# Kernel tuning notes

Hardware: AMD Instinct MI355X
Metric: run time of the kernel (lower is better)

## Reference

```python
import jax, jax.numpy as jnp
import numpy as np

EPS = 1e-12  # torch F.normalize eps

def l2norm(x, axis):
    n = jnp.sqrt(jnp.sum(x * x, axis=axis, keepdims=True))
    return x / jnp.maximum(n, EPS)

def setup_inputs() -> dict:
    key = jax.random.key(0)
    k1, k2, k3, k4 = jax.random.split(key, 4)
    N, C, H, W, K = 128, 128, 64, 64, 64
    x = jax.random.normal(k1, (N, C, H, W), dtype=jnp.float32)
    conv_w = jax.random.normal(k2, (K, C), dtype=jnp.float32) * 0.1
    conv_b = jax.random.normal(k3, (K,), dtype=jnp.float32) * 0.1
    centroids = jax.random.uniform(k4, (K, C), dtype=jnp.float32)
    return {"x": x, "conv_w": conv_w, "conv_b": conv_b, "centroids": centroids}

def reference(x, conv_w, conv_b, centroids):
    N, C, H, W = x.shape
    K = centroids.shape[0]
    xf = x.reshape(N, C, H * W)               # [N, C, S]
    xf = l2norm(xf, axis=1)                   # normalize_input over channels
    # 1x1 conv -> logits [N, K, S], softmax over clusters
    logits = jnp.einsum('ncs,kc->nks', xf, conv_w) + conv_b[None, :, None]
    a = jax.nn.softmax(logits, axis=1)        # [N, K, S]
    # VLAD: sum_s a[n,k,s]*(x[n,:,s] - c[k]) = (a @ x^T) - (sum_s a) * c
    vlad = jnp.einsum('nks,ncs->nkc', a, xf) - a.sum(axis=-1)[:, :, None] * centroids[None]
    vlad = l2norm(vlad, axis=2)               # intra-normalization
    vlad = vlad.reshape(N, K * C)
    return l2norm(vlad, axis=1)
```

## Files before the change

### kernel.cpp

```cpp
#include <hip/hip_runtime.h>
#include <math.h>

#define N_IMG 128
#define C_DIM 128
#define K_CL  64
#define S_PIX 4096
#define PB    4
#define SPB   (S_PIX/PB)
#define CHK   32
#define NCHK  (SPB/CHK)
#define NBUF  4

typedef __attribute__((ext_vector_type(8))) short bf16x8;
typedef __attribute__((ext_vector_type(4))) float f32x4;

__device__ __forceinline__ unsigned short f2bf_rn(float v) {
    unsigned u = __float_as_uint(v);
    unsigned r = u + 0x7fffu + ((u >> 16) & 1u);
    return (unsigned short)(r >> 16);
}
__device__ __forceinline__ float bf2f(unsigned short h) {
    return __uint_as_float(((unsigned)h) << 16);
}

__device__ __forceinline__ int sx(int c) { return ((c & 3) | ((c & 1) << 2)) & 7; }
__device__ __forceinline__ int sa(int k) { return (k >> 2) & 3; }

__device__ __forceinline__ void cvt8(const float* v, bf16x8& h, bf16x8& l) {
    union { unsigned w[4]; bf16x8 v8; } H, L;
    #pragma unroll
    for (int p = 0; p < 4; ++p) {
        unsigned u0 = __float_as_uint(v[2*p]);
        unsigned u1 = __float_as_uint(v[2*p+1]);
        float r0 = v[2*p]   - __uint_as_float(u0 & 0xffff0000u);
        float r1 = v[2*p+1] - __uint_as_float(u1 & 0xffff0000u);
        H.w[p] = __builtin_amdgcn_perm(u1, u0, 0x07060302u);
        L.w[p] = __builtin_amdgcn_perm(__float_as_uint(r1), __float_as_uint(r0), 0x07060302u);
    }
    h = H.v8; l = L.v8;
}

__device__ __forceinline__ void gll16(const float* g, float* l) {
    __builtin_amdgcn_global_load_lds(
        (const __attribute__((address_space(1))) unsigned int*)(g),
        (__attribute__((address_space(3))) unsigned int*)(l),
        16, 0, 0);
}

__global__ void k_prep(const float* __restrict__ w, unsigned short* __restrict__ wf,
                       float4* __restrict__ out4, float4* __restrict__ asum4) {
    int i = blockIdx.x * 256 + threadIdx.x;
    f32x4 z = (f32x4)0.f;
    if (i < (N_IMG*K_CL*C_DIM)/4) out4[i] = *(float4*)&z;
    if (i < (N_IMG*K_CL)/4)       asum4[i] = *(float4*)&z;
    if (i < 8192) {
        int j = i & 7, l = (i >> 3) & 63, t = (i >> 9) & 3, m = (i >> 11) & 3;
        int k = 16*m + (l & 15);
        int c = 32*t + 4*j + (l >> 4);
        float v = w[k * C_DIM + c];
        unsigned short h = f2bf_rn(v);
        wf[i]        = h;
        wf[8192 + i] = f2bf_rn(v - bf2f(h));
    }
}

__global__ __launch_bounds__(256, 1)
void k_main(const float* __restrict__ x,
            const unsigned short* __restrict__ wf,
            const float* __restrict__ bias,
            float* __restrict__ vlad,
            float* __restrict__ asum)
{
    __shared__ float Xs[NBUF][C_DIM*CHK];
    __shared__ unsigned short aS[2*K_CL*CHK];
    __shared__ __align__(16) float redS[2][2][16];

    const int tid  = threadIdx.x;
    const int lane = tid & 63;
    const int wid  = tid >> 6;
    const int lc   = lane & 15;
    const int g    = lane >> 4;

    const int p  = wid & 1;
    const int mh = wid >> 1;
    const int px = p*16 + lc;
    const int cq = wid * 32;

    const int n  = blockIdx.x / PB;
    const int sp = blockIdx.x % PB;
    const float* xn = x + (size_t)n * (C_DIM * S_PIX) + sp * SPB;

    bf16x8 Wh[2][4], Wl[2][4];
    #pragma unroll
    for (int mm = 0; mm < 2; ++mm)
        #pragma unroll
        for (int t = 0; t < 4; ++t) {
            int m = 2*mh + mm;
            Wh[mm][t] = *(const bf16x8*)&wf[((m*4 + t)*64 + lane)*8];
            Wl[mm][t] = *(const bf16x8*)&wf[((16 + m*4 + t)*64 + lane)*8];
        }
    #pragma unroll
    for (int mm = 0; mm < 2; ++mm)
        #pragma unroll
        for (int t = 0; t < 4; ++t) {
            asm volatile("" : "+v"(Wh[mm][t]));
            asm volatile("" : "+v"(Wl[mm][t]));
        }
    f32x4 bias_r[2];
    #pragma unroll
    for (int mm = 0; mm < 2; ++mm)
        bias_r[mm] = *(const f32x4*)&bias[32*mh + 16*mm + 4*g];

    f32x4 accV[4][2];
    #pragma unroll
    for (int m = 0; m < 4; ++m) { accV[m][0] = (f32x4)0.f; accV[m][1] = (f32x4)0.f; }
    float asum_acc[8];
    #pragma unroll
    for (int i = 0; i < 8; ++i) asum_acc[i] = 0.f;

    const int eA  = g*32 + (((px >> 2) ^ sx(g)) << 2) + (px & 3);
    const int sxB = sx(lc);
    const int saB = sa(lc);
    const int ps  = g >> 1;
    const int sb  = (8*g) & 15;

    auto STAGE = [&](int t, float* Xbuf) {
        #pragma unroll
        for (int i2 = 0; i2 < 4; ++i2) {
            int rowblk = wid*32 + i2*8;
            int row = rowblk + (lane >> 3);
            const float* gp = xn + (size_t)row * S_PIX + t*CHK
                            + 4*((lane & 7) ^ sx(row));
            gll16(gp, &Xbuf[rowblk * 32]);
        }
    };

    STAGE(0, Xs[0]);
    STAGE(1, Xs[1]);
    STAGE(2, Xs[2]);
    asm volatile("s_waitcnt vmcnt(8)" ::: "memory");
    __builtin_amdgcn_s_barrier();
    __builtin_amdgcn_sched_barrier(0);

    for (int ch = 0; ch < NCHK; ++ch) {
        float* Xb = Xs[ch & (NBUF-1)];

        if (ch + 3 < NCHK) STAGE(ch + 3, Xs[(ch + 3) & (NBUF-1)]);

        float s0 = 0.f, s1 = 0.f, s2 = 0.f, s3 = 0.f;
        f32x4 accL[2];
        accL[0] = (f32x4)0.f; accL[1] = (f32x4)0.f;
        #pragma unroll
        for (int t = 0; t < 4; ++t) {
            float xv[8];
            #pragma unroll
            for (int j = 0; j < 8; ++j)
                xv[j] = Xb[eA + 1024*t + 128*j];
            s0 = fmaf(xv[0], xv[0], s0); s1 = fmaf(xv[1], xv[1], s1);
            s2 = fmaf(xv[2], xv[2], s2); s3 = fmaf(xv[3], xv[3], s3);
            s0 = fmaf(xv[4], xv[4], s0); s1 = fmaf(xv[5], xv[5], s1);
            s2 = fmaf(xv[6], xv[6], s2); s3 = fmaf(xv[7], xv[7], s3);
            bf16x8 xh, xl;
            cvt8(xv, xh, xl);
            #pragma unroll
            for (int mm = 0; mm < 2; ++mm) {
                accL[mm] = __builtin_amdgcn_mfma_f32_16x16x32_bf16(Wh[mm][t], xh, accL[mm], 0,0,0);
                accL[mm] = __builtin_amdgcn_mfma_f32_16x16x32_bf16(Wh[mm][t], xl, accL[mm], 0,0,0);
                accL[mm] = __builtin_amdgcn_mfma_f32_16x16x32_bf16(Wl[mm][t], xh, accL[mm], 0,0,0);
            }
        }
        float ss = (s0 + s1) + (s2 + s3);
        ss += __shfl_xor(ss, 16); ss += __shfl_xor(ss, 32);
        float rnorm = 1.0f / fmaxf(sqrtf(ss), 1e-12f);

        float e[8]; float sm = 0.f;
        #pragma unroll
        for (int mm = 0; mm < 2; ++mm)
            #pragma unroll
            for (int jj = 0; jj < 4; ++jj) {
                float t2 = __expf(fmaf(accL[mm][jj], rnorm, bias_r[mm][jj]));
                e[mm*4+jj] = t2;
                sm += t2;
            }
        sm += __shfl_xor(sm, 16); sm += __shfl_xor(sm, 32);
        if (g == 0) redS[p][mh][lc] = sm;

        #pragma unroll
        for (int mm = 0; mm < 2; ++mm)
            #pragma unroll
            for (int jj = 0; jj < 4; ++jj) {
                float ap = e[mm*4+jj] * rnorm;
                unsigned u = __float_as_uint(ap);
                float r = ap - __uint_as_float(u & 0xffff0000u);
                int k  = 32*mh + 16*mm + 4*g + jj;
                int ix = k*32 + (((px >> 3) ^ g) << 3) + (px & 7);
                aS[ix]        = (unsigned short)(u >> 16);
                aS[2048 + ix] = (unsigned short)(__float_as_uint(r) >> 16);
            }

        asm volatile("s_waitcnt lgkmcnt(0)" ::: "memory");
        __builtin_amdgcn_s_barrier();
        __builtin_amdgcn_sched_barrier(0);

        {
            float S = sm + redS[p][mh^1][lc];
            float coef = __builtin_amdgcn_rcpf(S);
            #pragma unroll
            for (int i = 0; i < 8; ++i) asum_acc[i] = fmaf(e[i], coef, asum_acc[i]);
        }

        {
            float4 u0 = *(const float4*)&redS[ps][0][sb];
            float4 u1 = *(const float4*)&redS[ps][0][sb+4];
            float4 v0 = *(const float4*)&redS[ps][1][sb];
            float4 v1 = *(const float4*)&redS[ps][1][sb+4];
            float cf[8] = {u0.x+v0.x, u0.y+v0.y, u0.z+v0.z, u0.w+v0.w,
                           u1.x+v1.x, u1.y+v1.y, u1.z+v1.z, u1.w+v1.w};
            #pragma unroll
            for (int j = 0; j < 8; ++j) cf[j] = __builtin_amdgcn_rcpf(cf[j]);

            bf16x8 Ah[4], Al[4];
            #pragma unroll
            for (int m = 0; m < 4; ++m) {
                int off = (16*m + lc)*32 + ((g ^ saB) << 3);
                Ah[m] = *(const bf16x8*)&aS[off];
                Al[m] = *(const bf16x8*)&aS[2048 + off];
            }
            #pragma unroll
            for (int nn = 0; nn < 2; ++nn) {
                int c  = cq + nn*16 + lc;
                int P0 = (2*g) ^ sxB;
                float4 f0 = *(const float4*)&Xb[c*32 + P0*4];
                float4 f1 = *(const float4*)&Xb[c*32 + (P0 ^ 1)*4];
                float xv[8] = {f0.x*cf[0], f0.y*cf[1], f0.z*cf[2], f0.w*cf[3],
                               f1.x*cf[4], f1.y*cf[5], f1.z*cf[6], f1.w*cf[7]};
                bf16x8 xh, xl;
                cvt8(xv, xh, xl);
                #pragma unroll
                for (int m = 0; m < 4; ++m) {
                    accV[m][nn] = __builtin_amdgcn_mfma_f32_16x16x32_bf16(Ah[m], xh, accV[m][nn], 0,0,0);
                    accV[m][nn] = __builtin_amdgcn_mfma_f32_16x16x32_bf16(Ah[m], xl, accV[m][nn], 0,0,0);
                    accV[m][nn] = __builtin_amdgcn_mfma_f32_16x16x32_bf16(Al[m], xh, accV[m][nn], 0,0,0);
                }
            }
        }

        if (ch + 1 < NCHK) {
            if (ch + 3 < NCHK)
                asm volatile("s_waitcnt vmcnt(8) lgkmcnt(0)" ::: "memory");
            else if (ch + 2 < NCHK)
                asm volatile("s_waitcnt vmcnt(4) lgkmcnt(0)" ::: "memory");
            else
                asm volatile("s_waitcnt vmcnt(0) lgkmcnt(0)" ::: "memory");
            __builtin_amdgcn_s_barrier();
            __builtin_amdgcn_sched_barrier(0);
        }
    }

    float* vb = vlad + (size_t)n * (K_CL * C_DIM);
    #pragma unroll
    for (int m = 0; m < 4; ++m)
        #pragma unroll
        for (int nn = 0; nn < 2; ++nn)
            #pragma unroll
            for (int jj = 0; jj < 4; ++jj)
                atomicAdd(&vb[(16*m + 4*g + jj)*C_DIM + cq + nn*16 + lc],
                          accV[m][nn][jj]);

    #pragma unroll
    for (int i = 0; i < 8; ++i) {
        float v = asum_acc[i];
        v += __shfl_xor(v, 1); v += __shfl_xor(v, 2);
        v += __shfl_xor(v, 4); v += __shfl_xor(v, 8);
        asum_acc[i] = v;
    }
    if (lc == 0) {
        #pragma unroll
        for (int mm = 0; mm < 2; ++mm)
            #pragma unroll
            for (int jj = 0; jj < 4; ++jj)
                atomicAdd(&asum[n*K_CL + 32*mh + 16*mm + 4*g + jj], asum_acc[mm*4+jj]);
    }
}

__global__ __launch_bounds__(256)
void k_final(float* __restrict__ vlad,
             const float* __restrict__ asum,
             const float* __restrict__ cent)
{
    __shared__ float v[K_CL * 132];
    __shared__ float red[K_CL][4];
    __shared__ float rin[K_CL];
    __shared__ float rtot_s;
    const int tid = threadIdx.x;
    const int n   = blockIdx.x;
    float* vb = vlad + (size_t)n * (K_CL * C_DIM);
    const float* as = asum + n * K_CL;

    for (int i4 = tid; i4 < (K_CL*C_DIM)/4; i4 += 256) {
        int k = i4 >> 5, c4 = i4 & 31;
        float4 a = *(const float4*)&vb[i4*4];
        float4 b = *(const float4*)&cent[i4*4];
        float ak = as[k];
        float4 r; r.x = a.x - ak*b.x; r.y = a.y - ak*b.y;
                  r.z = a.z - ak*b.z; r.w = a.w - ak*b.w;
        *(float4*)&v[k*132 + c4*4] = r;
    }
    __syncthreads();
    {
        int k = tid >> 2, p = tid & 3;
        float s2 = 0.f;
        #pragma unroll
        for (int u = 0; u < 32; ++u) { float t = v[k*132 + (u<<2) + p]; s2 = fmaf(t, t, s2); }
        red[k][p] = s2;
    }
    __syncthreads();
    if (tid < K_CL) {
        float s2 = red[tid][0] + red[tid][1] + red[tid][2] + red[tid][3];
        float r  = 1.0f / fmaxf(sqrtf(s2), 1e-12f);
        rin[tid] = r;
        red[tid][0] = s2 * r * r;
    }
    __syncthreads();
    if (tid < 64) {
        float t = red[tid][0];
        t += __shfl_xor(t, 32); t += __shfl_xor(t, 16); t += __shfl_xor(t, 8);
        t += __shfl_xor(t, 4);  t += __shfl_xor(t, 2);  t += __shfl_xor(t, 1);
        if (tid == 0) rtot_s = 1.0f / fmaxf(sqrtf(t), 1e-12f);
    }
    __syncthreads();
    float rt = rtot_s;
    for (int i4 = tid; i4 < (K_CL*C_DIM)/4; i4 += 256) {
        int k = i4 >> 5, c4 = i4 & 31;
        float4 a = *(const float4*)&v[k*132 + c4*4];
        float s = rin[k] * rt;
        float4 r; r.x = a.x*s; r.y = a.y*s; r.z = a.z*s; r.w = a.w*s;
        *(float4*)&vb[i4*4] = r;
    }
}

extern "C" void kernel_launch(void* const* d_in, const int* in_sizes, int n_in,
                              void* d_out, int out_size, void* d_ws, size_t ws_size,
                              hipStream_t stream) {
    const float* x    = (const float*)d_in[0];
    const float* w    = (const float*)d_in[1];
    const float* b    = (const float*)d_in[2];
    const float* cent = (const float*)d_in[3];
    float* out = (float*)d_out;
    unsigned short* wf = (unsigned short*)d_ws;
    float* asum = (float*)((char*)d_ws + 32768);

    k_prep<<<(N_IMG*K_CL*C_DIM/4 + 255)/256, 256, 0, stream>>>(
        w, wf, (float4*)out, (float4*)asum);
    k_main<<<N_IMG * PB, 256, 0, stream>>>(x, wf, b, out, asum);
    k_final<<<N_IMG, 256, 0, stream>>>(out, asum, cent);
}
```

Before: 105.2 us.

## Replace atomic VLAD accumulation with per-block partial buffers reduced in final kernel

Each main-kernel block now writes its partial VLAD and assignment-sum accumulators to its own workspace slice with plain vector stores, instead of issuing scalar atomicAdds into the output. The final kernel sums the four spatial partials per image and undoes the MFMA fragment layout while subtracting the centroid term. This also removes the zero-initialisation of the output and asum from the prep kernel, which now only runs 32 blocks. The cost is extra workspace traffic, about 4x the VLAD size written and then read back, and a scattered LDS write pattern in the final kernel.

```diff
diff --git a/kernel.cpp b/kernel.cpp
--- a/kernel.cpp
+++ b/kernel.cpp
@@ -47,29 +47,23 @@
         16, 0, 0);
 }
 
-__global__ void k_prep(const float* __restrict__ w, unsigned short* __restrict__ wf,
-                       float4* __restrict__ out4, float4* __restrict__ asum4) {
+__global__ void k_prep(const float* __restrict__ w, unsigned short* __restrict__ wf) {
     int i = blockIdx.x * 256 + threadIdx.x;
-    f32x4 z = (f32x4)0.f;
-    if (i < (N_IMG*K_CL*C_DIM)/4) out4[i] = *(float4*)&z;
-    if (i < (N_IMG*K_CL)/4)       asum4[i] = *(float4*)&z;
-    if (i < 8192) {
-        int j = i & 7, l = (i >> 3) & 63, t = (i >> 9) & 3, m = (i >> 11) & 3;
-        int k = 16*m + (l & 15);
-        int c = 32*t + 4*j + (l >> 4);
-        float v = w[k * C_DIM + c];
-        unsigned short h = f2bf_rn(v);
-        wf[i]        = h;
-        wf[8192 + i] = f2bf_rn(v - bf2f(h));
-    }
+    int j = i & 7, l = (i >> 3) & 63, t = (i >> 9) & 3, m = (i >> 11) & 3;
+    int k = 16*m + (l & 15);
+    int c = 32*t + 4*j + (l >> 4);
+    float v = w[k * C_DIM + c];
+    unsigned short h = f2bf_rn(v);
+    wf[i]        = h;
+    wf[8192 + i] = f2bf_rn(v - bf2f(h));
 }
 
 __global__ __launch_bounds__(256, 1)
 void k_main(const float* __restrict__ x,
             const unsigned short* __restrict__ wf,
             const float* __restrict__ bias,
-            float* __restrict__ vlad,
-            float* __restrict__ asum)
+            float* __restrict__ pvlad,
+            float* __restrict__ pasum)
 {
     __shared__ float Xs[NBUF][C_DIM*CHK];
     __shared__ unsigned short aS[2*K_CL*CHK];
@@ -257,15 +251,12 @@
         }
     }
 
-    float* vb = vlad + (size_t)n * (K_CL * C_DIM);
+    float* pv = pvlad + (size_t)blockIdx.x * (K_CL * C_DIM);
     #pragma unroll
     for (int m = 0; m < 4; ++m)
         #pragma unroll
         for (int nn = 0; nn < 2; ++nn)
-            #pragma unroll
-            for (int jj = 0; jj < 4; ++jj)
-                atomicAdd(&vb[(16*m + 4*g + jj)*C_DIM + cq + nn*16 + lc],
-                          accV[m][nn][jj]);
+            *(float4*)&pv[wid*2048 + (m*2+nn)*256 + lane*4] = *(float4*)&accV[m][nn];
 
     #pragma unroll
     for (int i = 0; i < 8; ++i) {
@@ -275,44 +266,66 @@
         asum_acc[i] = v;
     }
     if (lc == 0) {
+        float* pa = pasum + (size_t)blockIdx.x * K_CL;
         #pragma unroll
         for (int mm = 0; mm < 2; ++mm)
             #pragma unroll
             for (int jj = 0; jj < 4; ++jj)
-                atomicAdd(&asum[n*K_CL + 32*mh + 16*mm + 4*g + jj], asum_acc[mm*4+jj]);
+                pa[32*mh + 16*mm + 4*g + jj] = asum_acc[mm*4+jj];
     }
 }
 
 __global__ __launch_bounds__(256)
-void k_final(float* __restrict__ vlad,
-             const float* __restrict__ asum,
-             const float* __restrict__ cent)
+void k_final(const float* __restrict__ pvlad,
+             const float* __restrict__ pasum,
+             const float* __restrict__ cent,
+             float* __restrict__ out)
 {
     __shared__ float v[K_CL * 132];
     __shared__ float red[K_CL][4];
     __shared__ float rin[K_CL];
+    __shared__ float fin_asum[K_CL];
     __shared__ float rtot_s;
     const int tid = threadIdx.x;
     const int n   = blockIdx.x;
-    float* vb = vlad + (size_t)n * (K_CL * C_DIM);
-    const float* as = asum + n * K_CL;
-
-    for (int i4 = tid; i4 < (K_CL*C_DIM)/4; i4 += 256) {
-        int k = i4 >> 5, c4 = i4 & 31;
-        float4 a = *(const float4*)&vb[i4*4];
-        float4 b = *(const float4*)&cent[i4*4];
-        float ak = as[k];
-        float4 r; r.x = a.x - ak*b.x; r.y = a.y - ak*b.y;
-                  r.z = a.z - ak*b.z; r.w = a.w - ak*b.w;
-        *(float4*)&v[k*132 + c4*4] = r;
+    const float* p0 = pvlad + (size_t)(n*PB + 0) * (K_CL*C_DIM);
+    const float* p1 = pvlad + (size_t)(n*PB + 1) * (K_CL*C_DIM);
+    const float* p2 = pvlad + (size_t)(n*PB + 2) * (K_CL*C_DIM);
+    const float* p3 = pvlad + (size_t)(n*PB + 3) * (K_CL*C_DIM);
+
+    if (tid < K_CL) {
+        const float* pa = pasum + (size_t)n * PB * K_CL;
+        fin_asum[tid] = (pa[tid] + pa[K_CL + tid])
+                      + (pa[2*K_CL + tid] + pa[3*K_CL + tid]);
+    }
+    __syncthreads();
+
+    for (int fq = tid; fq < (K_CL*C_DIM)/4; fq += 256) {
+        int f = fq * 4;
+        float4 a = *(const float4*)&p0[f];
+        float4 b = *(const float4*)&p1[f];
+        float4 c4 = *(const float4*)&p2[f];
+        float4 d = *(const float4*)&p3[f];
+        int wid  = f >> 11;
+        int mnn  = (f >> 8) & 7;
+        int m    = mnn >> 1, nn = mnn & 1;
+        int lane = (f >> 2) & 63;
+        int gg   = lane >> 4, lcc = lane & 15;
+        int kb   = 16*m + 4*gg;
+        int c    = wid*32 + nn*16 + lcc;
+        float sv[4] = {(a.x+b.x)+(c4.x+d.x), (a.y+b.y)+(c4.y+d.y),
+                       (a.z+b.z)+(c4.z+d.z), (a.w+b.w)+(c4.w+d.w)};
+        #pragma unroll
+        for (int jj = 0; jj < 4; ++jj)
+            v[(kb+jj)*132 + c] = sv[jj] - fin_asum[kb+jj] * cent[(kb+jj)*C_DIM + c];
     }
     __syncthreads();
     {
-        int k = tid >> 2, p = tid & 3;
+        int k = tid >> 2, pp = tid & 3;
         float s2 = 0.f;
         #pragma unroll
-        for (int u = 0; u < 32; ++u) { float t = v[k*132 + (u<<2) + p]; s2 = fmaf(t, t, s2); }
-        red[k][p] = s2;
+        for (int u = 0; u < 32; ++u) { float t = v[k*132 + (u<<2) + pp]; s2 = fmaf(t, t, s2); }
+        red[k][pp] = s2;
     }
     __syncthreads();
     if (tid < K_CL) {
@@ -330,12 +343,13 @@
     }
     __syncthreads();
     float rt = rtot_s;
+    float* ob = out + (size_t)n * (K_CL * C_DIM);
     for (int i4 = tid; i4 < (K_CL*C_DIM)/4; i4 += 256) {
         int k = i4 >> 5, c4 = i4 & 31;
         float4 a = *(const float4*)&v[k*132 + c4*4];
         float s = rin[k] * rt;
         float4 r; r.x = a.x*s; r.y = a.y*s; r.z = a.z*s; r.w = a.w*s;
-        *(float4*)&vb[i4*4] = r;
+        *(float4*)&ob[i4*4] = r;
     }
 }
 
@@ -348,10 +362,10 @@
     const float* cent = (const float*)d_in[3];
     float* out = (float*)d_out;
     unsigned short* wf = (unsigned short*)d_ws;
-    float* asum = (float*)((char*)d_ws + 32768);
-
-    k_prep<<<(N_IMG*K_CL*C_DIM/4 + 255)/256, 256, 0, stream>>>(
-        w, wf, (float4*)out, (float4*)asum);
-    k_main<<<N_IMG * PB, 256, 0, stream>>>(x, wf, b, out, asum);
-    k_final<<<N_IMG, 256, 0, stream>>>(out, asum, cent);
-}
+    float* pasum = (float*)((char*)d_ws + 32768);
+    float* pvlad = (float*)((char*)d_ws + 32768 + 131072);
+
+    k_prep<<<32, 256, 0, stream>>>(w, wf);
+    k_main<<<N_IMG * PB, 256, 0, stream>>>(x, wf, b, pvlad, pasum);
+    k_final<<<N_IMG, 256, 0, stream>>>(pvlad, pasum, cent, out);
+}
```

Measured after the change: 108.4 us. +3.0%, slower.

## Software-pipeline logits phase of next chunk with VLAD phase of current chunk

Applied to the files above, without the earlier changes.

Splits the per-chunk work into a logits/softmax phase (PHASE_A) and a VLAD accumulation phase. It interleaves them so that phase A for chunk ch+1 runs alongside phase B for chunk ch, using double-buffered assignment and reduction buffers. This removes one barrier per chunk and lets the MFMA work of the two phases overlap. In exchange the X staging ring shrinks from 4 to 3 buffers with prefetch distance 2, each iteration now waits with vmcnt(0), and register pressure rises from carrying e values across iterations.

```diff
diff --git a/kernel.cpp b/kernel.cpp
--- a/kernel.cpp
+++ b/kernel.cpp
@@ -9,7 +9,6 @@
 #define SPB   (S_PIX/PB)
 #define CHK   32
 #define NCHK  (SPB/CHK)
-#define NBUF  4
 
 typedef __attribute__((ext_vector_type(8))) short bf16x8;
 typedef __attribute__((ext_vector_type(4))) float f32x4;
@@ -71,9 +70,9 @@
             float* __restrict__ vlad,
             float* __restrict__ asum)
 {
-    __shared__ float Xs[NBUF][C_DIM*CHK];
-    __shared__ unsigned short aS[2*K_CL*CHK];
-    __shared__ __align__(16) float redS[2][2][16];
+    __shared__ float Xs[3][C_DIM*CHK];
+    __shared__ unsigned short aS[2*2*2048];
+    __shared__ __align__(16) float redS[2][2][2][16];
 
     const int tid  = threadIdx.x;
     const int lane = tid & 63;
@@ -135,18 +134,7 @@
         }
     };
 
-    STAGE(0, Xs[0]);
-    STAGE(1, Xs[1]);
-    STAGE(2, Xs[2]);
-    asm volatile("s_waitcnt vmcnt(8)" ::: "memory");
-    __builtin_amdgcn_s_barrier();
-    __builtin_amdgcn_sched_barrier(0);
-
-    for (int ch = 0; ch < NCHK; ++ch) {
-        float* Xb = Xs[ch & (NBUF-1)];
-
-        if (ch + 3 < NCHK) STAGE(ch + 3, Xs[(ch + 3) & (NBUF-1)]);
-
+    auto PHASE_A = [&](const float* Xa, int gen, float* eOut, float& smOut) {
         float s0 = 0.f, s1 = 0.f, s2 = 0.f, s3 = 0.f;
         f32x4 accL[2];
         accL[0] = (f32x4)0.f; accL[1] = (f32x4)0.f;
@@ -155,7 +143,7 @@
             float xv[8];
             #pragma unroll
             for (int j = 0; j < 8; ++j)
-                xv[j] = Xb[eA + 1024*t + 128*j];
+                xv[j] = Xa[eA + 1024*t + 128*j];
             s0 = fmaf(xv[0], xv[0], s0); s1 = fmaf(xv[1], xv[1], s1);
             s2 = fmaf(xv[2], xv[2], s2); s3 = fmaf(xv[3], xv[3], s3);
             s0 = fmaf(xv[4], xv[4], s0); s1 = fmaf(xv[5], xv[5], s1);
@@ -173,65 +161,91 @@
         ss += __shfl_xor(ss, 16); ss += __shfl_xor(ss, 32);
         float rnorm = 1.0f / fmaxf(sqrtf(ss), 1e-12f);
 
-        float e[8]; float sm = 0.f;
+        float sm = 0.f;
         #pragma unroll
         for (int mm = 0; mm < 2; ++mm)
             #pragma unroll
             for (int jj = 0; jj < 4; ++jj) {
                 float t2 = __expf(fmaf(accL[mm][jj], rnorm, bias_r[mm][jj]));
-                e[mm*4+jj] = t2;
+                eOut[mm*4+jj] = t2;
                 sm += t2;
             }
         sm += __shfl_xor(sm, 16); sm += __shfl_xor(sm, 32);
-        if (g == 0) redS[p][mh][lc] = sm;
-
+        if (g == 0) redS[gen][p][mh][lc] = sm;
+        smOut = sm;
+
+        unsigned short* aW = aS + gen*4096;
         #pragma unroll
         for (int mm = 0; mm < 2; ++mm)
             #pragma unroll
             for (int jj = 0; jj < 4; ++jj) {
-                float ap = e[mm*4+jj] * rnorm;
+                float ap = eOut[mm*4+jj] * rnorm;
                 unsigned u = __float_as_uint(ap);
                 float r = ap - __uint_as_float(u & 0xffff0000u);
                 int k  = 32*mh + 16*mm + 4*g + jj;
                 int ix = k*32 + (((px >> 3) ^ g) << 3) + (px & 7);
-                aS[ix]        = (unsigned short)(u >> 16);
-                aS[2048 + ix] = (unsigned short)(__float_as_uint(r) >> 16);
-            }
-
-        asm volatile("s_waitcnt lgkmcnt(0)" ::: "memory");
-        __builtin_amdgcn_s_barrier();
-        __builtin_amdgcn_sched_barrier(0);
+                aW[ix]        = (unsigned short)(u >> 16);
+                aW[2048 + ix] = (unsigned short)(__float_as_uint(r) >> 16);
+            }
+    };
+
+    float eP[8], smP;
+
+    STAGE(0, Xs[0]);
+    STAGE(1, Xs[1]);
+    asm volatile("s_waitcnt vmcnt(4)" ::: "memory");
+    __builtin_amdgcn_s_barrier();
+    __builtin_amdgcn_sched_barrier(0);
+
+    PHASE_A(Xs[0], 0, eP, smP);
+    STAGE(2, Xs[2]);
+    asm volatile("s_waitcnt vmcnt(4) lgkmcnt(0)" ::: "memory");
+    __builtin_amdgcn_s_barrier();
+    __builtin_amdgcn_sched_barrier(0);
+
+    float* bufB = Xs[0];
+    float* bufA = Xs[1];
+    float* bufS = Xs[2];
+
+    for (int ch = 0; ch < NCHK; ++ch) {
+        if (ch >= 1 && ch + 2 < NCHK) STAGE(ch + 2, bufS);
+
+        const int genC = ch & 1;
 
         {
-            float S = sm + redS[p][mh^1][lc];
+            float S = smP + redS[genC][p][mh^1][lc];
             float coef = __builtin_amdgcn_rcpf(S);
             #pragma unroll
-            for (int i = 0; i < 8; ++i) asum_acc[i] = fmaf(e[i], coef, asum_acc[i]);
-        }
+            for (int i = 0; i < 8; ++i) asum_acc[i] = fmaf(eP[i], coef, asum_acc[i]);
+        }
+
+        float eN[8], smN;
+        if (ch + 1 < NCHK) PHASE_A(bufA, (ch + 1) & 1, eN, smN);
 
         {
-            float4 u0 = *(const float4*)&redS[ps][0][sb];
-            float4 u1 = *(const float4*)&redS[ps][0][sb+4];
-            float4 v0 = *(const float4*)&redS[ps][1][sb];
-            float4 v1 = *(const float4*)&redS[ps][1][sb+4];
+            float4 u0 = *(const float4*)&redS[genC][ps][0][sb];
+            float4 u1 = *(const float4*)&redS[genC][ps][0][sb+4];
+            float4 v0 = *(const float4*)&redS[genC][ps][1][sb];
+            float4 v1 = *(const float4*)&redS[genC][ps][1][sb+4];
             float cf[8] = {u0.x+v0.x, u0.y+v0.y, u0.z+v0.z, u0.w+v0.w,
                            u1.x+v1.x, u1.y+v1.y, u1.z+v1.z, u1.w+v1.w};
             #pragma unroll
             for (int j = 0; j < 8; ++j) cf[j] = __builtin_amdgcn_rcpf(cf[j]);
 
+            const unsigned short* aR = aS + genC*4096;
             bf16x8 Ah[4], Al[4];
             #pragma unroll
             for (int m = 0; m < 4; ++m) {
                 int off = (16*m + lc)*32 + ((g ^ saB) << 3);
-                Ah[m] = *(const bf16x8*)&aS[off];
-                Al[m] = *(const bf16x8*)&aS[2048 + off];
+                Ah[m] = *(const bf16x8*)&aR[off];
+                Al[m] = *(const bf16x8*)&aR[2048 + off];
             }
             #pragma unroll
             for (int nn = 0; nn < 2; ++nn) {
                 int c  = cq + nn*16 + lc;
                 int P0 = (2*g) ^ sxB;
-                float4 f0 = *(const float4*)&Xb[c*32 + P0*4];
-                float4 f1 = *(const float4*)&Xb[c*32 + (P0 ^ 1)*4];
+                float4 f0 = *(const float4*)&bufB[c*32 + P0*4];
+                float4 f1 = *(const float4*)&bufB[c*32 + (P0 ^ 1)*4];
                 float xv[8] = {f0.x*cf[0], f0.y*cf[1], f0.z*cf[2], f0.w*cf[3],
                                f1.x*cf[4], f1.y*cf[5], f1.z*cf[6], f1.w*cf[7]};
                 bf16x8 xh, xl;
@@ -246,15 +260,15 @@
         }
 
         if (ch + 1 < NCHK) {
-            if (ch + 3 < NCHK)
-                asm volatile("s_waitcnt vmcnt(8) lgkmcnt(0)" ::: "memory");
-            else if (ch + 2 < NCHK)
-                asm volatile("s_waitcnt vmcnt(4) lgkmcnt(0)" ::: "memory");
-            else
-                asm volatile("s_waitcnt vmcnt(0) lgkmcnt(0)" ::: "memory");
+            asm volatile("s_waitcnt vmcnt(0) lgkmcnt(0)" ::: "memory");
             __builtin_amdgcn_s_barrier();
             __builtin_amdgcn_sched_barrier(0);
         }
+
+        float* t0 = bufB; bufB = bufA; bufA = bufS; bufS = t0;
+        #pragma unroll
+        for (int i = 0; i < 8; ++i) eP[i] = eN[i];
+        smP = smN;
     }
 
     float* vb = vlad + (size_t)n * (K_CL * C_DIM);
@@ -308,11 +322,11 @@
     }
     __syncthreads();
     {
-        int k = tid >> 2, p = tid & 3;
+        int k = tid >> 2, pp = tid & 3;
         float s2 = 0.f;
         #pragma unroll
-        for (int u = 0; u < 32; ++u) { float t = v[k*132 + (u<<2) + p]; s2 = fmaf(t, t, s2); }
-        red[k][p] = s2;
+        for (int u = 0; u < 32; ++u) { float t = v[k*132 + (u<<2) + pp]; s2 = fmaf(t, t, s2); }
+        red[k][pp] = s2;
     }
     __syncthreads();
     if (tid < K_CL) {
```

After: 108.2 us. 2.8% more time.
